# Kernel tuning notes

Measured on AMD Instinct MI355X. Metric: run time of the kernel, lower is better.

Reference implementation:

```python
import jax, jax.numpy as jnp
import numpy as np

Q = 400          # num queries
P = 200000       # num points in event
N_INST = 100     # num GT instances
ALPHA = 0.25     # focal alpha
GAMMA = 2.0      # focal gamma
COST_MASK_W = 1.0
COST_DICE_W = 1.0


def setup_inputs() -> dict:
    key = jax.random.key(0)
    k1, k2 = jax.random.split(key)
    pred_masks = jax.random.normal(k1, (Q, P), dtype=jnp.float32)
    labels = jax.random.randint(k2, (P,), 0, N_INST, dtype=jnp.int64 if jax.config.jax_enable_x64 else jnp.int32)
    return {"pred_masks": pred_masks, "labels": labels, "num_instances": N_INST}


def reference(pred_masks, labels, num_instances):
    # pred_masks: [Q, P] mask logits; labels: [P] instance ids in [0, num_instances)
    x = pred_masks.astype(jnp.float32)
    p = jax.nn.sigmoid(x)                      # [Q, P]
    log_p = jax.nn.log_sigmoid(x)              # log sigmoid(x), stable
    log_1mp = jax.nn.log_sigmoid(-x)           # log(1 - sigmoid(x)), stable

    # Focal BCE per point, split by binary target value t in {0,1}:
    #   t=1: alpha     * (1-p)^gamma * (-log p)
    #   t=0: (1-alpha) *    p^gamma  * (-log(1-p))
    f1 = -ALPHA * (1.0 - p) ** GAMMA * log_p        # [Q, P]
    f0 = -(1.0 - ALPHA) * p ** GAMMA * log_1mp      # [Q, P]

    # One-hot GT masks per instance: T[p, j] = 1 iff labels[p] == j
    T = jax.nn.one_hot(labels, num_instances, dtype=jnp.float32)  # [P, N]

    # cost_mask[q, j] = mean_p [ T[p,j]*f1[q,p] + (1-T[p,j])*f0[q,p] ]
    #                 = ( (f1 - f0) @ T + sum_p f0 ) / P   -- avoids [Q,N,P]
    Pn = jnp.asarray(x.shape[1], dtype=jnp.float32)
    cost_mask = (jnp.einsum('qp,pj->qj', f1 - f0, T) + f0.sum(-1, keepdims=True)) / Pn

    # Dice cost (same einsum form as the torch code)
    counts = T.sum(0)                                # [N] points per instance
    numerator = 2.0 * jnp.einsum('qp,pj->qj', p, T)  # [Q, N]
    denominator = p.sum(-1)[:, None] + counts[None, :]
    cost_dice = 1.0 - (numerator + 1.0) / (denominator + 1.0)

    return COST_MASK_W * cost_mask + COST_DICE_W * cost_dice  # [Q, N]
```

## Files before the change

kernel.cpp:

```cpp
#include <hip/hip_runtime.h>
#include <cstdint>


#define FOCAL_ALPHA 0.25f
constexpr int NMAX   = 128;
constexpr int NTILES = 7;
constexpr int BLOCK  = 256;
constexpr int KC     = 146;

typedef __attribute__((ext_vector_type(8))) short short8;
typedef __attribute__((ext_vector_type(4))) float f32x4;
typedef __attribute__((ext_vector_type(2))) float f32x2;

union BU { uint4 q; short8 v; uint32_t u[4]; };

__device__ __forceinline__ void point_math2(f32x2 x, f32x2& d, f32x2& f0o, f32x2& po) {
    f32x2 t = x * (-1.44269504089f);
    f32x2 e;
    e.x = __builtin_amdgcn_exp2f(t.x);
    e.y = __builtin_amdgcn_exp2f(t.y);
    f32x2 a = e + 1.0f;
    f32x2 p;
    p.x = __builtin_amdgcn_rcpf(a.x);
    p.y = __builtin_amdgcn_rcpf(a.y);
    f32x2 L;
    L.x = __builtin_amdgcn_logf(a.x);
    L.y = __builtin_amdgcn_logf(a.y);
    f32x2 l  = L * 0.69314718056f;
    f32x2 lm = L * (-0.69314718056f) - x;
    f32x2 om = e * p;
    f32x2 f1 = (om * om) * (l * FOCAL_ALPHA);
    f32x2 f0 = (p * p) * (lm * -(1.0f - FOCAL_ALPHA));
    d   = f1 - f0;
    f0o = f0;
    po  = p;
}

__device__ __forceinline__ uint32_t pack_bf16_trunc(float lo, float hi) {
    return __builtin_amdgcn_perm(__float_as_uint(hi), __float_as_uint(lo), 0x07060302u);
}

__global__ __launch_bounds__(BLOCK, 4) void
matcher_main(const float* __restrict__ pred, const int* __restrict__ labels,
             float* __restrict__ S1, float* __restrict__ S2,
             float* __restrict__ sumf0, float* __restrict__ sump,
             int Q, int P, int N) {
    __shared__ uint4 Bl[2][NTILES][64];

    const int tid  = threadIdx.x;
    const int wave = tid >> 6;
    const int lane = tid & 63;
    const int m    = lane & 15;
    const int quad = lane >> 4;

    const int strip = blockIdx.y * 4 + wave;
    const int q0    = strip * 16;
    const bool alive = (q0 < Q);

    const int total_steps = P >> 5;
    const int per         = (total_steps + KC - 1) / KC;
    const int s0          = blockIdx.x * per;
    const int s1          = min(s0 + per, total_steps);
    if (s0 >= s1) return;
    const int nsteps = s1 - s0;

    const int  t0   = wave;
    const int  t1   = wave + 4;
    const bool has2 = (t1 < NTILES);
    const int  tgt0 = t0 * 16 + m;
    const int  tgt1 = t1 * 16 + m;

    const int*   lr = labels + (size_t)s0 * 32 + quad * 8;
    const float* pr = pred + (size_t)(q0 + m) * P + quad * 8 + (size_t)s0 * 32;

    f32x4 c1[NTILES], c2[NTILES];
    #pragma unroll
    for (int t = 0; t < NTILES; ++t) {
        c1[t] = (f32x4){0.f, 0.f, 0.f, 0.f};
        c2[t] = (f32x4){0.f, 0.f, 0.f, 0.f};
    }
    f32x2 sf2 = (f32x2){0.f, 0.f};
    f32x2 sp2 = (f32x2){0.f, 0.f};

    auto build = [&](int4 l0, int4 l1, int buf) {
        const int ls[8] = {l0.x, l0.y, l0.z, l0.w, l1.x, l1.y, l1.z, l1.w};
        BU B0;
        #pragma unroll
        for (int i = 0; i < 4; ++i) {
            uint32_t lo = (ls[2*i]   == tgt0) ? 0x00003F80u : 0u;
            uint32_t hi = (ls[2*i+1] == tgt0) ? 0x3F800000u : 0u;
            B0.u[i] = lo | hi;
        }
        Bl[buf][t0][lane] = B0.q;
        if (has2) {
            BU B1;
            #pragma unroll
            for (int i = 0; i < 4; ++i) {
                uint32_t lo = (ls[2*i]   == tgt1) ? 0x00003F80u : 0u;
                uint32_t hi = (ls[2*i+1] == tgt1) ? 0x3F800000u : 0u;
                B1.u[i] = lo | hi;
            }
            Bl[buf][t1][lane] = B1.q;
        }
    };

    {
        int4 a0 = *(const int4*)lr;
        int4 a1 = *(const int4*)(lr + 4);
        build(a0, a1, 0);
    }
    int4 cl0 = (int4){0,0,0,0}, cl1 = (int4){0,0,0,0};
    if (nsteps > 1) {
        lr += 32;
        cl0 = *(const int4*)lr;
        cl1 = *(const int4*)(lr + 4);
    }
    float4 cx0, cx1;
    if (alive) {
        cx0 = *(const float4*)pr;
        cx1 = *(const float4*)(pr + 4);
    }
    __syncthreads();

    int ph = 0;
    for (int s = 0; s < nsteps; ++s) {
        const bool more = (s + 1 < nsteps);

        float4 nx0, nx1;
        if (alive && more) {
            nx0 = *(const float4*)(pr + 32);
            nx1 = *(const float4*)(pr + 36);
        }

        if (alive) {
            BU A1, A2;
            const f32x2 xp[4] = {(f32x2){cx0.x, cx0.y}, (f32x2){cx0.z, cx0.w},
                                 (f32x2){cx1.x, cx1.y}, (f32x2){cx1.z, cx1.w}};
            #pragma unroll
            for (int i = 0; i < 4; ++i) {
                f32x2 d2, f02, p2;
                point_math2(xp[i], d2, f02, p2);
                sf2 += f02;
                sp2 += p2;
                A1.u[i] = pack_bf16_trunc(d2.x, d2.y);
                A2.u[i] = pack_bf16_trunc(p2.x, p2.y);
            }

            #pragma unroll
            for (int t = 0; t < NTILES; ++t) {
                BU B;
                B.q = Bl[ph][t][lane];
                c1[t] = __builtin_amdgcn_mfma_f32_16x16x32_bf16(A1.v, B.v, c1[t], 0, 0, 0);
                c2[t] = __builtin_amdgcn_mfma_f32_16x16x32_bf16(A2.v, B.v, c2[t], 0, 0, 0);
            }
            pr += 32;
            cx0 = nx0; cx1 = nx1;
        }

        if (more) {
            build(cl0, cl1, ph ^ 1);
            lr += 32;
            if (s + 2 < nsteps) {
                cl0 = *(const int4*)lr;
                cl1 = *(const int4*)(lr + 4);
            }
        }
        __syncthreads();
        ph ^= 1;
    }

    if (alive) {
        float a = sf2.x + sf2.y;
        float b = sp2.x + sp2.y;
        a += __shfl_xor(a, 16, 64);
        a += __shfl_xor(a, 32, 64);
        b += __shfl_xor(b, 16, 64);
        b += __shfl_xor(b, 32, 64);
        if (lane < 16) {
            unsafeAtomicAdd(&sumf0[q0 + lane], a);
            unsafeAtomicAdd(&sump[q0 + lane], b);
        }

        #pragma unroll
        for (int t = 0; t < NTILES; ++t) {
            const int col = t * 16 + m;
            if (col < N) {
                #pragma unroll
                for (int r = 0; r < 4; ++r) {
                    const int row = q0 + quad * 4 + r;
                    unsafeAtomicAdd(&S1[(size_t)row * N + col], c1[t][r]);
                    unsafeAtomicAdd(&S2[(size_t)row * N + col], c2[t][r]);
                }
            }
        }
    }
}

__global__ __launch_bounds__(256) void
matcher_counts(const int* __restrict__ labels, int* __restrict__ counts, int P, int N) {
    __shared__ int c[NMAX];
    for (int i = threadIdx.x; i < NMAX; i += 256) c[i] = 0;
    __syncthreads();
    const int stride = gridDim.x * 256;
    for (int i = blockIdx.x * 256 + threadIdx.x; i < P; i += stride)
        atomicAdd(&c[labels[i]], 1);
    __syncthreads();
    for (int j = threadIdx.x; j < N; j += 256)
        if (c[j] != 0) atomicAdd(&counts[j], c[j]);
}

__global__ __launch_bounds__(256) void
matcher_final(const float* __restrict__ S1, const float* __restrict__ S2,
              const float* __restrict__ sumf0, const float* __restrict__ sump,
              const int* __restrict__ counts, float* __restrict__ out,
              int Q, int P, int N) {
    int idx = blockIdx.x * 256 + threadIdx.x;
    if (idx >= Q * N) return;
    int q = idx / N;
    int j = idx - q * N;
    float invP = 1.0f / (float)P;
    float cost_mask = (S1[idx] + sumf0[q]) * invP;
    float cost_dice = 1.0f - (2.0f * S2[idx] + 1.0f) / (sump[q] + (float)counts[j] + 1.0f);
    out[idx] = cost_mask + cost_dice;
}

extern "C" void kernel_launch(void* const* d_in, const int* in_sizes, int n_in,
                              void* d_out, int out_size, void* d_ws, size_t ws_size,
                              hipStream_t stream) {
    const float* pred   = (const float*)d_in[0];
    const int*   labels = (const int*)d_in[1];
    const int P = in_sizes[1];
    const int Q = in_sizes[0] / P;
    const int N = out_size / Q;

    float* S1     = (float*)d_ws;
    float* S2     = S1 + (size_t)Q * N;
    float* sumf0  = S2 + (size_t)Q * N;
    float* sump   = sumf0 + Q;
    int*   counts = (int*)(sump + Q);
    size_t base_bytes = ((size_t)2 * Q * N + 2 * Q + N) * sizeof(float);

    hipMemsetAsync(d_ws, 0, base_bytes, stream);
    matcher_counts<<<64, 256, 0, stream>>>(labels, counts, P, N);

    const int strips = (Q + 15) / 16;
    dim3 grid(KC, (strips + 3) / 4);
    matcher_main<<<grid, BLOCK, 0, stream>>>(pred, labels, S1, S2, sumf0, sump, Q, P, N);

    int qn = Q * N;
    matcher_final<<<(qn + 255) / 256, 256, 0, stream>>>(S1, S2, sumf0, sump, counts,
                                                        (float*)d_out, Q, P, N);
}
```

Before: 517.2 us.

## Replace global atomic accumulation with per-chunk partials and a dedicated reduce kernel

Instead of every block atomically adding its 16x112 MFMA tiles into S1/S2, each block now writes its partial tiles (S1 in fp32, S2 in fp16) to a workspace slice indexed by K-chunk. A new 1024-thread reduce kernel sums the chunks and fuses the final cost computation, which removes the S1/S2 memset and the final kernel. The loop barrier is also changed to a plain LDS-wait plus s_barrier instead of __syncthreads. This avoids heavy atomic contention, at the cost of extra workspace traffic and fp16 rounding of the dice partials. The old atomic path is kept as a fallback when the workspace is too small.

Result: faster. 469.4 us (-9.2%).

```diff
diff --git a/kernel.cpp b/kernel.cpp
--- a/kernel.cpp
+++ b/kernel.cpp
@@ -1,4 +1,5 @@
 #include <hip/hip_runtime.h>
+#include <hip/hip_fp16.h>
 #include <cstdint>
 
 
@@ -12,7 +13,13 @@
 typedef __attribute__((ext_vector_type(4))) float f32x4;
 typedef __attribute__((ext_vector_type(2))) float f32x2;
 
-union BU { uint4 q; short8 v; uint32_t u[4]; };
+union BU  { uint4 q; short8 v; uint32_t u[4]; };
+union H2U { __half2 h; uint32_t u; };
+
+__device__ __forceinline__ void block_sync_lgkm() {
+    asm volatile("s_waitcnt lgkmcnt(0)" ::: "memory");
+    __builtin_amdgcn_s_barrier();
+}
 
 __device__ __forceinline__ void point_math2(f32x2 x, f32x2& d, f32x2& f0o, f32x2& po) {
     f32x2 t = x * (-1.44269504089f);
@@ -40,11 +47,12 @@
     return __builtin_amdgcn_perm(__float_as_uint(hi), __float_as_uint(lo), 0x07060302u);
 }
 
+template<bool PART>
 __global__ __launch_bounds__(BLOCK, 4) void
 matcher_main(const float* __restrict__ pred, const int* __restrict__ labels,
-             float* __restrict__ S1, float* __restrict__ S2,
+             float* __restrict__ P1, uint32_t* __restrict__ P2,
              float* __restrict__ sumf0, float* __restrict__ sump,
-             int Q, int P, int N) {
+             int Q, int P, int N, int nstr) {
     __shared__ uint4 Bl[2][NTILES][64];
 
     const int tid  = threadIdx.x;
@@ -58,10 +66,25 @@
     const bool alive = (q0 < Q);
 
     const int total_steps = P >> 5;
-    const int per         = (total_steps + KC - 1) / KC;
+    const int per         = (total_steps + gridDim.x - 1) / gridDim.x;
     const int s0          = blockIdx.x * per;
     const int s1          = min(s0 + per, total_steps);
-    if (s0 >= s1) return;
+
+    if (s0 >= s1) {
+        if constexpr (PART) {
+            if (alive) {
+                const size_t tb = ((size_t)blockIdx.x * nstr + strip) * NTILES;
+                float4* o1 = (float4*)P1 + tb * 64 + lane;
+                uint2*  o2 = (uint2*)P2  + tb * 64 + lane;
+                #pragma unroll
+                for (int t = 0; t < NTILES; ++t) {
+                    o1[t * 64] = make_float4(0.f, 0.f, 0.f, 0.f);
+                    o2[t * 64] = make_uint2(0u, 0u);
+                }
+            }
+        }
+        return;
+    }
     const int nsteps = s1 - s0;
 
     const int  t0   = wave;
@@ -120,7 +143,7 @@
         cx0 = *(const float4*)pr;
         cx1 = *(const float4*)(pr + 4);
     }
-    __syncthreads();
+    block_sync_lgkm();
 
     int ph = 0;
     for (int s = 0; s < nsteps; ++s) {
@@ -165,7 +188,7 @@
                 cl1 = *(const int4*)(lr + 4);
             }
         }
-        __syncthreads();
+        block_sync_lgkm();
         ph ^= 1;
     }
 
@@ -181,17 +204,71 @@
             unsafeAtomicAdd(&sump[q0 + lane], b);
         }
 
-        #pragma unroll
-        for (int t = 0; t < NTILES; ++t) {
-            const int col = t * 16 + m;
-            if (col < N) {
-                #pragma unroll
-                for (int r = 0; r < 4; ++r) {
-                    const int row = q0 + quad * 4 + r;
-                    unsafeAtomicAdd(&S1[(size_t)row * N + col], c1[t][r]);
-                    unsafeAtomicAdd(&S2[(size_t)row * N + col], c2[t][r]);
+        if constexpr (PART) {
+            const size_t tb = ((size_t)blockIdx.x * nstr + strip) * NTILES;
+            float4* o1 = (float4*)P1 + tb * 64 + lane;
+            uint2*  o2 = (uint2*)P2  + tb * 64 + lane;
+            #pragma unroll
+            for (int t = 0; t < NTILES; ++t) {
+                o1[t * 64] = make_float4(c1[t][0], c1[t][1], c1[t][2], c1[t][3]);
+                H2U ha, hb;
+                ha.h = __floats2half2_rn(c2[t][0], c2[t][1]);
+                hb.h = __floats2half2_rn(c2[t][2], c2[t][3]);
+                o2[t * 64] = make_uint2(ha.u, hb.u);
+            }
+        } else {
+            float* S1 = P1;
+            float* S2 = (float*)P2;
+            #pragma unroll
+            for (int t = 0; t < NTILES; ++t) {
+                const int col = t * 16 + m;
+                if (col < N) {
+                    #pragma unroll
+                    for (int r = 0; r < 4; ++r) {
+                        const int row = q0 + quad * 4 + r;
+                        unsafeAtomicAdd(&S1[(size_t)row * N + col], c1[t][r]);
+                        unsafeAtomicAdd(&S2[(size_t)row * N + col], c2[t][r]);
+                    }
                 }
             }
+        }
+    }
+}
+
+__global__ __launch_bounds__(1024) void
+matcher_reduce(const float* __restrict__ P1, const uint32_t* __restrict__ P2,
+               const float* __restrict__ sumf0, const float* __restrict__ sump,
+               const int* __restrict__ counts, float* __restrict__ out,
+               int Q, int P, int N, int nstr, int kc) {
+    __shared__ float R1[4][256];
+    __shared__ float R2[4][256];
+    const int tid   = threadIdx.x;
+    const int ks    = tid >> 8;
+    const int el    = tid & 255;
+    const int t     = blockIdx.x;
+    const int strip = blockIdx.y;
+    const int lane  = el >> 2;
+    const int r     = el & 3;
+
+    float a1 = 0.f, a2 = 0.f;
+    for (int k = ks; k < kc; k += 4) {
+        const size_t tb = ((size_t)k * nstr + strip) * NTILES + t;
+        a1 += P1[tb * 256 + el];
+        H2U h; h.u = P2[tb * 128 + lane * 2 + (r >> 1)];
+        a2 += (r & 1) ? __high2float(h.h) : __low2float(h.h);
+    }
+    R1[ks][el] = a1;
+    R2[ks][el] = a2;
+    __syncthreads();
+    if (tid < 256) {
+        a1 = R1[0][el] + R1[1][el] + R1[2][el] + R1[3][el];
+        a2 = R2[0][el] + R2[1][el] + R2[2][el] + R2[3][el];
+        const int q = strip * 16 + (lane >> 4) * 4 + r;
+        const int j = t * 16 + (lane & 15);
+        if (q < Q && j < N) {
+            float cost_mask = (a1 + sumf0[q]) / (float)P;
+            float cost_dice = 1.0f - (2.0f * a2 + 1.0f) / (sump[q] + (float)counts[j] + 1.0f);
+            out[q * N + j] = cost_mask + cost_dice;
         }
     }
 }
@@ -233,21 +310,40 @@
     const int Q = in_sizes[0] / P;
     const int N = out_size / Q;
 
-    float* S1     = (float*)d_ws;
-    float* S2     = S1 + (size_t)Q * N;
-    float* sumf0  = S2 + (size_t)Q * N;
+    const int total_steps = P >> 5;
+    const int strips = (Q + 15) / 16;
+    const int nyb    = (strips + 3) / 4;
+    const int nstr   = nyb * 4;
+
+    float* sumf0  = (float*)d_ws;
     float* sump   = sumf0 + Q;
     int*   counts = (int*)(sump + Q);
-    size_t base_bytes = ((size_t)2 * Q * N + 2 * Q + N) * sizeof(float);
-
-    hipMemsetAsync(d_ws, 0, base_bytes, stream);
+    size_t hdr = (((size_t)(2 * Q + N)) * sizeof(float) + 255) & ~(size_t)255;
+
+    size_t perkc = (size_t)nstr * NTILES * (256 * 4 + 128 * 4);
+    int kcmax = (ws_size > hdr) ? (int)((ws_size - hdr) / perkc) : 0;
+    int kc = KC < kcmax ? KC : kcmax;
+    if (kc > total_steps) kc = total_steps;
+    const bool part = (kc >= 8);
+
+    hipMemsetAsync(d_ws, 0, (size_t)(2 * Q + N) * sizeof(float), stream);
     matcher_counts<<<64, 256, 0, stream>>>(labels, counts, P, N);
 
-    const int strips = (Q + 15) / 16;
-    dim3 grid(KC, (strips + 3) / 4);
-    matcher_main<<<grid, BLOCK, 0, stream>>>(pred, labels, S1, S2, sumf0, sump, Q, P, N);
-
-    int qn = Q * N;
-    matcher_final<<<(qn + 255) / 256, 256, 0, stream>>>(S1, S2, sumf0, sump, counts,
-                                                        (float*)d_out, Q, P, N);
-}
+    if (part) {
+        float*    P1 = (float*)((char*)d_ws + hdr);
+        uint32_t* P2 = (uint32_t*)(P1 + (size_t)kc * nstr * NTILES * 256);
+        matcher_main<true><<<dim3(kc, nyb), BLOCK, 0, stream>>>(
+            pred, labels, P1, P2, sumf0, sump, Q, P, N, nstr);
+        matcher_reduce<<<dim3(NTILES, strips), 1024, 0, stream>>>(
+            P1, P2, sumf0, sump, counts, (float*)d_out, Q, P, N, nstr, kc);
+    } else {
+        float* S1 = (float*)((char*)d_ws + hdr);
+        float* S2 = S1 + (size_t)Q * N;
+        hipMemsetAsync(S1, 0, (size_t)2 * Q * N * sizeof(float), stream);
+        int kca = KC < total_steps ? KC : total_steps;
+        matcher_main<false><<<dim3(kca, nyb), BLOCK, 0, stream>>>(
+            pred, labels, S1, (uint32_t*)S2, sumf0, sump, Q, P, N, nstr);
+        matcher_final<<<(Q * N + 255) / 256, 256, 0, stream>>>(
+            S1, S2, sumf0, sump, counts, (float*)d_out, Q, P, N);
+    }
+}
```
